# Performance work log

Measured on AMD Instinct MI355X. Metric: run time of the kernel, lower is better.

The kernel has to match this reference:

```python
import jax, jax.numpy as jnp
import numpy as np

N_NODES = 100000
N_EDGES = 1600000
IN_CH = 128
HID = 32
HEADS = 4
OUT_CH = 32
NEG_SLOPE = 0.2  # PyG GATConv default


def _gat_conv(x, src, dst, W, a_src, a_dst, bias, concat):
    """One GATConv layer (eval mode, self-loops already in src/dst).
    x: [N, F_in], W: [F_in, H*C], a_src/a_dst: [H, C], bias: [H*C] or [C].
    """
    N = x.shape[0]
    H, C = a_src.shape
    h = (x @ W).reshape(N, H, C)                      # [N, H, C]
    alpha_s = jnp.einsum('nhc,hc->nh', h, a_src)      # [N, H]
    alpha_d = jnp.einsum('nhc,hc->nh', h, a_dst)      # [N, H]
    logits = jax.nn.leaky_relu(alpha_s[src] + alpha_d[dst], NEG_SLOPE)  # [E, H]
    # segment softmax over incoming edges of each destination node
    m = jax.ops.segment_max(logits, dst, num_segments=N)   # [N, H]
    e = jnp.exp(logits - m[dst])                            # [E, H]
    denom = jax.ops.segment_sum(e, dst, num_segments=N)     # [N, H]
    alpha = e / denom[dst]                                   # [E, H]
    msg = h[src] * alpha[:, :, None]                         # [E, H, C]
    out = jax.ops.segment_sum(msg, dst, num_segments=N)     # [N, H, C]
    out = out.reshape(N, H * C) if concat else out.mean(axis=1)
    return out + bias


def setup_inputs() -> dict:
    key = jax.random.key(0)
    ks = jax.random.split(key, 12)
    x = jax.random.normal(ks[0], (N_NODES, IN_CH), dtype=jnp.float32)
    edge_index = jax.random.randint(ks[1], (2, N_EDGES), 0, N_NODES, dtype=jnp.int64)
    g = 0.1  # glorot-ish scale
    W1 = jax.random.normal(ks[2], (IN_CH, HEADS * HID), dtype=jnp.float32) * g
    a_src1 = jax.random.normal(ks[3], (HEADS, HID), dtype=jnp.float32) * g
    a_dst1 = jax.random.normal(ks[4], (HEADS, HID), dtype=jnp.float32) * g
    b1 = jnp.zeros((HEADS * HID,), dtype=jnp.float32)
    W2 = jax.random.normal(ks[5], (HEADS * HID, OUT_CH), dtype=jnp.float32) * g
    a_src2 = jax.random.normal(ks[6], (1, OUT_CH), dtype=jnp.float32) * g
    a_dst2 = jax.random.normal(ks[7], (1, OUT_CH), dtype=jnp.float32) * g
    b2 = jnp.zeros((OUT_CH,), dtype=jnp.float32)
    return {"x": x, "edge_index": edge_index,
            "W1": W1, "a_src1": a_src1, "a_dst1": a_dst1, "b1": b1,
            "W2": W2, "a_src2": a_src2, "a_dst2": a_dst2, "b2": b2}


def reference(x, edge_index, W1, a_src1, a_dst1, b1, W2, a_src2, a_dst2, b2):
    N = x.shape[0]
    loops = jnp.arange(N, dtype=edge_index.dtype)
    src = jnp.concatenate([edge_index[0], loops])  # add self-loops (PyG default)
    dst = jnp.concatenate([edge_index[1], loops])
    h = _gat_conv(x, src, dst, W1, a_src1, a_dst1, b1, concat=True)   # [N, H*HID]
    h = jax.nn.elu(h)
    out = _gat_conv(h, src, dst, W2, a_src2, a_dst2, b2, concat=False)  # [N, OUT]
    return out
```

## Files before the change

kernel.cpp:

```cpp
#include <hip/hip_runtime.h>
#include <math.h>

#define N_NODES 100000
#define N_EDGES 1600000
#define E_TOT   1700000
#define NEG_SLOPE 0.2f
#define NBUCK 196
#define G1_BLOCKS 1563
#define HISTB_BLOCKS 831

typedef unsigned short ushort_t;
typedef unsigned int uint_t;
typedef __attribute__((ext_vector_type(8))) short bf16x8;
typedef __attribute__((ext_vector_type(4))) float f32x4;

__device__ __forceinline__ float lrelu(float v) { return v > 0.f ? v : NEG_SLOPE * v; }
__device__ __forceinline__ float bf16lo(uint_t u) { return __uint_as_float(u << 16); }
__device__ __forceinline__ float bf16hi(uint_t u) { return __uint_as_float(u & 0xffff0000u); }
__device__ __forceinline__ ushort_t f2bf(float f) {
    uint_t u = __float_as_uint(f);
    u += 0x7fffu + ((u >> 16) & 1u);
    return (ushort_t)(u >> 16);
}

union BU { uint4 u; bf16x8 b; };

__global__ __launch_bounds__(256) void k_prep(const float* __restrict__ W,
                                              ushort_t* __restrict__ Wb,
                                              int* __restrict__ bucket_cnt)
{
    const int idx = blockIdx.x * 256 + threadIdx.x;
    if (blockIdx.x == 0 && threadIdx.x <= NBUCK) bucket_cnt[threadIdx.x] = 0;
    const int j  = idx & 7;
    const int kq = (idx >> 3) & 3;
    const int n  = (idx >> 5) & 15;
    const int tc = (idx >> 9) & 7;
    const int kc = idx >> 12;
    const int k = kc * 32 + kq * 8 + j;
    const int col = tc * 16 + n;
    Wb[idx] = f2bf(W[k * 128 + col]);
}

__global__ __launch_bounds__(256) void k_gemm1_histB(const float* __restrict__ x,
                                                     const ushort_t* __restrict__ Wb,
                                                     const float* __restrict__ a_src,
                                                     const float* __restrict__ a_dst,
                                                     ushort_t* __restrict__ hb,
                                                     float* __restrict__ as_,
                                                     float* __restrict__ ad_,
                                                     const int* __restrict__ ei,
                                                     int* __restrict__ bucket_cnt)
{
    __shared__ int lbin[NBUCK];
    const int t = threadIdx.x;

    if (blockIdx.x >= G1_BLOCKS) {
        const int e0 = (blockIdx.x - G1_BLOCKS) * 2048 + t;
        for (int i = t; i < NBUCK; i += 256) lbin[i] = 0;
        __syncthreads();
#pragma unroll
        for (int i = 0; i < 8; ++i) {
            const int e = e0 + i * 256;
            if (e < E_TOT) {
                const int d = (e < N_EDGES) ? ei[N_EDGES + e] : (e - N_EDGES);
                atomicAdd(&lbin[d >> 9], 1);
            }
        }
        __syncthreads();
        for (int i = t; i < NBUCK; i += 256)
            if (lbin[i]) atomicAdd(&bucket_cnt[i], lbin[i]);
        return;
    }

    const int lane = t & 63;
    const int w = t >> 6;
    const int rbase = blockIdx.x * 64 + w * 16;
    const int li = lane & 15;
    const int g = lane >> 4;

    f32x4 acc[8];
#pragma unroll
    for (int tc = 0; tc < 8; ++tc) acc[tc] = (f32x4){0.f, 0.f, 0.f, 0.f};

    int arow = rbase + li;
    if (arow > N_NODES - 1) arow = N_NODES - 1;
    const float* xr = x + (size_t)arow * 128 + g * 8;

#pragma unroll
    for (int kc = 0; kc < 4; ++kc) {
        const float4 a0 = *(const float4*)(xr + kc * 32);
        const float4 a1 = *(const float4*)(xr + kc * 32 + 4);
        BU au;
        au.u.x = (uint_t)f2bf(a0.x) | ((uint_t)f2bf(a0.y) << 16);
        au.u.y = (uint_t)f2bf(a0.z) | ((uint_t)f2bf(a0.w) << 16);
        au.u.z = (uint_t)f2bf(a1.x) | ((uint_t)f2bf(a1.y) << 16);
        au.u.w = (uint_t)f2bf(a1.z) | ((uint_t)f2bf(a1.w) << 16);
        const bf16x8 af = au.b;
#pragma unroll
        for (int tc = 0; tc < 8; ++tc) {
            const bf16x8 bf = *(const bf16x8*)(Wb + (size_t)(kc * 8 + tc) * 512 + li * 32 + g * 8);
            acc[tc] = __builtin_amdgcn_mfma_f32_16x16x32_bf16(af, bf, acc[tc], 0, 0, 0);
        }
    }

#pragma unroll
    for (int r = 0; r < 4; ++r) {
        const int row = rbase + g * 4 + r;
        if (row < N_NODES) {
            ushort_t* hp = hb + (size_t)row * 128 + li;
#pragma unroll
            for (int tc = 0; tc < 8; ++tc) hp[tc * 16] = f2bf(acc[tc][r]);
        }
    }

    float asv[8], adv[8];
#pragma unroll
    for (int tc = 0; tc < 8; ++tc) {
        asv[tc] = a_src[tc * 16 + li];
        adv[tc] = a_dst[tc * 16 + li];
    }
#pragma unroll
    for (int h = 0; h < 4; ++h) {
#pragma unroll
        for (int r = 0; r < 4; ++r) {
            float ps = acc[2 * h][r] * asv[2 * h] + acc[2 * h + 1][r] * asv[2 * h + 1];
            float pd = acc[2 * h][r] * adv[2 * h] + acc[2 * h + 1][r] * adv[2 * h + 1];
            ps += __shfl_xor(ps, 1); pd += __shfl_xor(pd, 1);
            ps += __shfl_xor(ps, 2); pd += __shfl_xor(pd, 2);
            ps += __shfl_xor(ps, 4); pd += __shfl_xor(pd, 4);
            ps += __shfl_xor(ps, 8); pd += __shfl_xor(pd, 8);
            const int row = rbase + g * 4 + r;
            if (li == 0 && row < N_NODES) {
                as_[row * 4 + h] = ps;
                ad_[row * 4 + h] = pd;
            }
        }
    }
}

__global__ __launch_bounds__(256) void k_scanB(const int* __restrict__ bucket_cnt,
                                               int* __restrict__ bucket_base,
                                               int* __restrict__ bucket_cursor)
{
    __shared__ int s[256];
    const int t = threadIdx.x;
    const int v = (t < NBUCK) ? bucket_cnt[t] : 0;
    s[t] = v; __syncthreads();
    for (int off = 1; off < 256; off <<= 1) {
        int a = (t >= off) ? s[t - off] : 0;
        __syncthreads();
        s[t] += a;
        __syncthreads();
    }
    const int excl = s[t] - v;
    if (t < NBUCK) {
        bucket_base[t] = excl;
        bucket_cursor[t] = excl;
        if (t == NBUCK - 1) bucket_base[NBUCK] = excl + v;
    }
}

__global__ __launch_bounds__(256) void k_scatterB(const int* __restrict__ ei,
                                                  int* __restrict__ bucket_cursor,
                                                  uint2* __restrict__ pairs)
{
    __shared__ int lcnt[NBUCK];
    __shared__ int lbase[NBUCK];
    const int t = threadIdx.x;
    const int e0 = blockIdx.x * 2048 + t;

    for (int i = t; i < NBUCK; i += 256) lcnt[i] = 0;
    __syncthreads();

    int s8[8], d8[8];
#pragma unroll
    for (int i = 0; i < 8; ++i) {
        const int e = e0 + i * 256;
        int s = -1, d = 0;
        if (e < E_TOT) {
            if (e < N_EDGES) { s = ei[e]; d = ei[N_EDGES + e]; }
            else { s = d = e - N_EDGES; }
            atomicAdd(&lcnt[d >> 9], 1);
        }
        s8[i] = s; d8[i] = d;
    }
    __syncthreads();
    for (int i = t; i < NBUCK; i += 256) {
        const int c = lcnt[i];
        lbase[i] = (c > 0) ? atomicAdd(&bucket_cursor[i], c) : 0;
    }
    __syncthreads();
    for (int i = t; i < NBUCK; i += 256) lcnt[i] = 0;
    __syncthreads();
#pragma unroll
    for (int i = 0; i < 8; ++i) {
        if (s8[i] >= 0) {
            const int b = d8[i] >> 9;
            const int pos = lbase[b] + atomicAdd(&lcnt[b], 1);
            pairs[pos] = make_uint2((uint_t)s8[i], (uint_t)d8[i]);
        }
    }
}

__global__ __launch_bounds__(256) void k_buildC(const uint2* __restrict__ pairs,
                                                const int* __restrict__ bucket_base,
                                                int* __restrict__ row_ptr,
                                                int* __restrict__ col_src)
{
    __shared__ int cnt[512];
    __shared__ int cur[512];
    __shared__ int ps[256];
    const int b = blockIdx.x, t = threadIdx.x;
    const int bstart = bucket_base[b], bend = bucket_base[b + 1];
    const int node0 = b << 9;

    cnt[t] = 0; cnt[t + 256] = 0;
    __syncthreads();
    for (int e = bstart + t; e < bend; e += 256)
        atomicAdd(&cnt[pairs[e].y - node0], 1);
    __syncthreads();

    const int pa = cnt[2 * t], pb = cnt[2 * t + 1];
    ps[t] = pa + pb; __syncthreads();
    for (int off = 1; off < 256; off <<= 1) {
        int a = (t >= off) ? ps[t - off] : 0;
        __syncthreads();
        ps[t] += a;
        __syncthreads();
    }
    const int pe = bstart + ps[t] - (pa + pb);
    cur[2 * t] = pe;
    cur[2 * t + 1] = pe + pa;
    const int n0 = node0 + 2 * t, n1 = node0 + 2 * t + 1;
    if (n0 < N_NODES) row_ptr[n0] = pe;
    if (n1 < N_NODES) row_ptr[n1] = pe + pa;
    if (b == 0 && t == 0) row_ptr[N_NODES] = E_TOT;
    __syncthreads();

    for (int e = bstart + t; e < bend; e += 256) {
        const uint2 pr = pairs[e];
        const int pos = atomicAdd(&cur[pr.y - node0], 1);
        col_src[pos] = (int)pr.x;
    }
}

__global__ __launch_bounds__(64) void k_agg1(const ushort_t* __restrict__ hb,
                                             const float* __restrict__ as_,
                                             const float* __restrict__ ad_,
                                             const int* __restrict__ row_ptr,
                                             const int* __restrict__ col_src,
                                             const float* __restrict__ bias,
                                             ushort_t* __restrict__ x2b)
{
    __shared__ float sEx[256];
    __shared__ int sSrc[64];
    const int n = blockIdx.x;
    const int lane = threadIdx.x;
    const int start = row_ptr[n], end = row_ptr[n + 1];
    const float4 adv = *(const float4*)(ad_ + (size_t)n * 4);

    const int hsel = lane >> 4;
    const int c0 = lane * 2;
    float2 acc = make_float2(0.f, 0.f);
    float4 ds = make_float4(0.f, 0.f, 0.f, 0.f);
    for (int base = start; base < end; base += 64) {
        const int e = base + lane;
        const int cnt = min(64, end - base);
        float4 ex = make_float4(0.f, 0.f, 0.f, 0.f);
        int s = 0;
        if (e < end) {
            s = col_src[e];
            const float4 av = *(const float4*)(as_ + (size_t)s * 4);
            ex.x = __expf(lrelu(av.x + adv.x));
            ex.y = __expf(lrelu(av.y + adv.y));
            ex.z = __expf(lrelu(av.z + adv.z));
            ex.w = __expf(lrelu(av.w + adv.w));
            ds.x += ex.x; ds.y += ex.y; ds.z += ex.z; ds.w += ex.w;
        }
        __syncthreads();
        *(float4*)(sEx + lane * 4) = ex;
        sSrc[lane] = s;
        __syncthreads();
        for (int i = 0; i < cnt; ++i) {
            const float w = sEx[i * 4 + hsel];
            const uint_t hv = *(const uint_t*)(hb + (size_t)sSrc[i] * 128 + c0);
            acc.x = fmaf(w, bf16lo(hv), acc.x);
            acc.y = fmaf(w, bf16hi(hv), acc.y);
        }
    }
#pragma unroll
    for (int off = 32; off > 0; off >>= 1) {
        ds.x += __shfl_xor(ds.x, off);
        ds.y += __shfl_xor(ds.y, off);
        ds.z += __shfl_xor(ds.z, off);
        ds.w += __shfl_xor(ds.w, off);
    }
    const float denom = hsel == 0 ? ds.x : hsel == 1 ? ds.y : hsel == 2 ? ds.z : ds.w;
    float o0 = acc.x / denom + bias[c0];
    float o1 = acc.y / denom + bias[c0 + 1];
    o0 = o0 > 0.f ? o0 : __expf(o0) - 1.f;
    o1 = o1 > 0.f ? o1 : __expf(o1) - 1.f;
    const uint_t q0 = f2bf(o0), q1 = f2bf(o1);
    *(uint_t*)(x2b + (size_t)n * 128 + c0) = q0 | (q1 << 16);
}

__global__ __launch_bounds__(256) void k_gemm2(const ushort_t* __restrict__ x2b,
                                               const float* __restrict__ W,
                                               const float* __restrict__ a_src,
                                               const float* __restrict__ a_dst,
                                               ushort_t* __restrict__ hb2,
                                               float* __restrict__ as_,
                                               float* __restrict__ ad_)
{
    __shared__ float sW[128 * 32];
    const int t = threadIdx.x;
    {
        const float4* W4 = (const float4*)W;
        float4* s4 = (float4*)sW;
#pragma unroll
        for (int i = 0; i < 4; ++i) s4[t + 256 * i] = W4[t + 256 * i];
    }
    __syncthreads();

    const int rr = t >> 5;
    const int c = t & 31;
    const float a_s = a_src[c], a_d = a_dst[c];

    for (int g = 0; g < 8; ++g) {
        const int row = blockIdx.x * 64 + g * 8 + rr;
        if (row >= N_NODES) continue;
        const ushort_t* xp = x2b + (size_t)row * 128;

        float acc = 0.f;
        for (int k = 0; k < 128; k += 4) {
            const uint2 u = *(const uint2*)(xp + k);
            acc = fmaf(bf16lo(u.x), sW[(k + 0) * 32 + c], acc);
            acc = fmaf(bf16hi(u.x), sW[(k + 1) * 32 + c], acc);
            acc = fmaf(bf16lo(u.y), sW[(k + 2) * 32 + c], acc);
            acc = fmaf(bf16hi(u.y), sW[(k + 3) * 32 + c], acc);
        }

        hb2[(size_t)row * 32 + c] = f2bf(acc);
        float ps = acc * a_s, pd = acc * a_d;
#pragma unroll
        for (int off = 16; off > 0; off >>= 1) {
            ps += __shfl_xor(ps, off);
            pd += __shfl_xor(pd, off);
        }
        if (c == 0) { as_[row] = ps; ad_[row] = pd; }
    }
}

__global__ __launch_bounds__(64) void k_agg2(const ushort_t* __restrict__ hb2,
                                             const float* __restrict__ as_,
                                             const float* __restrict__ ad_,
                                             const int* __restrict__ row_ptr,
                                             const int* __restrict__ col_src,
                                             const float* __restrict__ bias,
                                             float* __restrict__ out)
{
    __shared__ float sEx[64];
    __shared__ int sSrc[64];
    const int n = blockIdx.x;
    const int lane = threadIdx.x;
    const int start = row_ptr[n], end = row_ptr[n + 1];
    const float adn = ad_[n];

    const int c = lane & 31, half = lane >> 5;
    float acc = 0.f, dsum = 0.f;
    for (int base = start; base < end; base += 64) {
        const int e = base + lane;
        const int cnt = min(64, end - base);
        float ex = 0.f; int s = 0;
        if (e < end) {
            s = col_src[e];
            ex = __expf(lrelu(as_[s] + adn));
            dsum += ex;
        }
        __syncthreads();
        sEx[lane] = ex;
        sSrc[lane] = s;
        __syncthreads();
        for (int i = half; i < cnt; i += 2) {
            const ushort_t u = hb2[(size_t)sSrc[i] * 32 + c];
            acc = fmaf(sEx[i], __uint_as_float((uint_t)u << 16), acc);
        }
    }
#pragma unroll
    for (int off = 32; off > 0; off >>= 1) dsum += __shfl_xor(dsum, off);
    acc += __shfl_xor(acc, 32);
    if (half == 0) out[(size_t)n * 32 + c] = acc / dsum + bias[c];
}

extern "C" void kernel_launch(void* const* d_in, const int* in_sizes, int n_in,
                              void* d_out, int out_size, void* d_ws, size_t ws_size,
                              hipStream_t stream)
{
    const float* x      = (const float*)d_in[0];
    const int*   ei     = (const int*)d_in[1];
    const float* W1     = (const float*)d_in[2];
    const float* a_src1 = (const float*)d_in[3];
    const float* a_dst1 = (const float*)d_in[4];
    const float* b1     = (const float*)d_in[5];
    const float* W2     = (const float*)d_in[6];
    const float* a_src2 = (const float*)d_in[7];
    const float* a_dst2 = (const float*)d_in[8];
    const float* b2     = (const float*)d_in[9];
    float* out = (float*)d_out;

    char* p = (char*)d_ws;
    auto alloc = [&](size_t bytes) { char* q = p; p += (bytes + 255) & ~(size_t)255; return q; };
    ushort_t* h1b = (ushort_t*)alloc((size_t)N_NODES * 128 * 2);
    ushort_t* x2b = (ushort_t*)alloc((size_t)N_NODES * 128 * 2);
    ushort_t* h2b = (ushort_t*)alloc((size_t)N_NODES * 32 * 2);
    ushort_t* Wb  = (ushort_t*)alloc((size_t)16384 * 2);
    float* as1    = (float*)alloc((size_t)N_NODES * 4 * 4);
    float* ad1    = (float*)alloc((size_t)N_NODES * 4 * 4);
    float* as2    = (float*)alloc((size_t)N_NODES * 4);
    float* ad2    = (float*)alloc((size_t)N_NODES * 4);
    int* row_ptr  = (int*)alloc((size_t)(N_NODES + 1) * 4);
    int* bucket_cnt    = (int*)alloc((NBUCK + 1) * 4);
    int* bucket_base   = (int*)alloc((NBUCK + 1) * 4);
    int* bucket_cursor = (int*)alloc((NBUCK + 1) * 4);
    uint2* pairs  = (uint2*)alloc((size_t)E_TOT * 8);
    int* col_src  = (int*)alloc((size_t)E_TOT * 4);

    k_prep<<<64, 256, 0, stream>>>(W1, Wb, bucket_cnt);
    k_gemm1_histB<<<G1_BLOCKS + HISTB_BLOCKS, 256, 0, stream>>>(
        x, Wb, a_src1, a_dst1, h1b, as1, ad1, ei, bucket_cnt);
    k_scanB<<<1, 256, 0, stream>>>(bucket_cnt, bucket_base, bucket_cursor);
    k_scatterB<<<HISTB_BLOCKS, 256, 0, stream>>>(ei, bucket_cursor, pairs);
    k_buildC<<<NBUCK, 256, 0, stream>>>(pairs, bucket_base, row_ptr, col_src);
    k_agg1<<<N_NODES, 64, 0, stream>>>(h1b, as1, ad1, row_ptr, col_src, b1, x2b);
    k_gemm2<<<(N_NODES + 63) / 64, 256, 0, stream>>>(x2b, W2, a_src2, a_dst2, h2b, as2, ad2);
    k_agg2<<<N_NODES, 64, 0, stream>>>(h2b, as2, ad2, row_ptr, col_src, b2, out);
}
```

Measured before the change: 273.1 us.

## Fuse edge scatter into gemm1 launch and widen aggregation loads

The bucket histogram and scan now run as separate kernels ahead of gemm1, so the scatter pass can share a launch with gemm1 and overlap with it instead of running as its own kernel afterwards. The bucket counter is cleared with a memset. Both aggregation kernels now split edges across lane groups and load wider bf16 vectors per lane, followed by cross-lane shuffle reductions. This trades some extra shuffles and an extra small launch for fewer dependent serialized passes and better per-lane memory throughput.

```diff
diff --git a/kernel.cpp b/kernel.cpp
--- a/kernel.cpp
+++ b/kernel.cpp
@@ -7,7 +7,7 @@
 #define NEG_SLOPE 0.2f
 #define NBUCK 196
 #define G1_BLOCKS 1563
-#define HISTB_BLOCKS 831
+#define SCAT_BLOCKS 831
 
 typedef unsigned short ushort_t;
 typedef unsigned int uint_t;
@@ -25,12 +25,53 @@
 
 union BU { uint4 u; bf16x8 b; };
 
+__global__ __launch_bounds__(256) void k_histC(const int* __restrict__ ei,
+                                               int* __restrict__ bucket_cnt)
+{
+    __shared__ int lbin[NBUCK];
+    const int t = threadIdx.x;
+    const int e0 = blockIdx.x * 2048 + t;
+    for (int i = t; i < NBUCK; i += 256) lbin[i] = 0;
+    __syncthreads();
+#pragma unroll
+    for (int i = 0; i < 8; ++i) {
+        const int e = e0 + i * 256;
+        if (e < E_TOT) {
+            const int d = (e < N_EDGES) ? ei[N_EDGES + e] : (e - N_EDGES);
+            atomicAdd(&lbin[d >> 9], 1);
+        }
+    }
+    __syncthreads();
+    for (int i = t; i < NBUCK; i += 256)
+        if (lbin[i]) atomicAdd(&bucket_cnt[i], lbin[i]);
+}
+
+__global__ __launch_bounds__(256) void k_scanB(const int* __restrict__ bucket_cnt,
+                                               int* __restrict__ bucket_base,
+                                               int* __restrict__ bucket_cursor)
+{
+    __shared__ int s[256];
+    const int t = threadIdx.x;
+    const int v = (t < NBUCK) ? bucket_cnt[t] : 0;
+    s[t] = v; __syncthreads();
+    for (int off = 1; off < 256; off <<= 1) {
+        int a = (t >= off) ? s[t - off] : 0;
+        __syncthreads();
+        s[t] += a;
+        __syncthreads();
+    }
+    const int excl = s[t] - v;
+    if (t < NBUCK) {
+        bucket_base[t] = excl;
+        bucket_cursor[t] = excl;
+        if (t == NBUCK - 1) bucket_base[NBUCK] = excl + v;
+    }
+}
+
 __global__ __launch_bounds__(256) void k_prep(const float* __restrict__ W,
-                                              ushort_t* __restrict__ Wb,
-                                              int* __restrict__ bucket_cnt)
+                                              ushort_t* __restrict__ Wb)
 {
     const int idx = blockIdx.x * 256 + threadIdx.x;
-    if (blockIdx.x == 0 && threadIdx.x <= NBUCK) bucket_cnt[threadIdx.x] = 0;
     const int j  = idx & 7;
     const int kq = (idx >> 3) & 3;
     const int n  = (idx >> 5) & 15;
@@ -41,34 +82,53 @@
     Wb[idx] = f2bf(W[k * 128 + col]);
 }
 
-__global__ __launch_bounds__(256) void k_gemm1_histB(const float* __restrict__ x,
-                                                     const ushort_t* __restrict__ Wb,
-                                                     const float* __restrict__ a_src,
-                                                     const float* __restrict__ a_dst,
-                                                     ushort_t* __restrict__ hb,
-                                                     float* __restrict__ as_,
-                                                     float* __restrict__ ad_,
-                                                     const int* __restrict__ ei,
-                                                     int* __restrict__ bucket_cnt)
-{
-    __shared__ int lbin[NBUCK];
+__global__ __launch_bounds__(256) void k_gemm1_scat(const float* __restrict__ x,
+                                                    const ushort_t* __restrict__ Wb,
+                                                    const float* __restrict__ a_src,
+                                                    const float* __restrict__ a_dst,
+                                                    ushort_t* __restrict__ hb,
+                                                    float* __restrict__ as_,
+                                                    float* __restrict__ ad_,
+                                                    const int* __restrict__ ei,
+                                                    int* __restrict__ bucket_cursor,
+                                                    uint2* __restrict__ pairs)
+{
+    __shared__ int lcnt[NBUCK];
+    __shared__ int lbase[NBUCK];
     const int t = threadIdx.x;
 
     if (blockIdx.x >= G1_BLOCKS) {
         const int e0 = (blockIdx.x - G1_BLOCKS) * 2048 + t;
-        for (int i = t; i < NBUCK; i += 256) lbin[i] = 0;
-        __syncthreads();
+        for (int i = t; i < NBUCK; i += 256) lcnt[i] = 0;
+        __syncthreads();
+        int s8[8], d8[8];
 #pragma unroll
         for (int i = 0; i < 8; ++i) {
             const int e = e0 + i * 256;
+            int s = -1, d = 0;
             if (e < E_TOT) {
-                const int d = (e < N_EDGES) ? ei[N_EDGES + e] : (e - N_EDGES);
-                atomicAdd(&lbin[d >> 9], 1);
+                if (e < N_EDGES) { s = ei[e]; d = ei[N_EDGES + e]; }
+                else { s = d = e - N_EDGES; }
+                atomicAdd(&lcnt[d >> 9], 1);
             }
-        }
-        __syncthreads();
-        for (int i = t; i < NBUCK; i += 256)
-            if (lbin[i]) atomicAdd(&bucket_cnt[i], lbin[i]);
+            s8[i] = s; d8[i] = d;
+        }
+        __syncthreads();
+        for (int i = t; i < NBUCK; i += 256) {
+            const int c = lcnt[i];
+            lbase[i] = (c > 0) ? atomicAdd(&bucket_cursor[i], c) : 0;
+        }
+        __syncthreads();
+        for (int i = t; i < NBUCK; i += 256) lcnt[i] = 0;
+        __syncthreads();
+#pragma unroll
+        for (int i = 0; i < 8; ++i) {
+            if (s8[i] >= 0) {
+                const int b = d8[i] >> 9;
+                const int pos = lbase[b] + atomicAdd(&lcnt[b], 1);
+                pairs[pos] = make_uint2((uint_t)s8[i], (uint_t)d8[i]);
+            }
+        }
         return;
     }
 
@@ -138,70 +198,6 @@
     }
 }
 
-__global__ __launch_bounds__(256) void k_scanB(const int* __restrict__ bucket_cnt,
-                                               int* __restrict__ bucket_base,
-                                               int* __restrict__ bucket_cursor)
-{
-    __shared__ int s[256];
-    const int t = threadIdx.x;
-    const int v = (t < NBUCK) ? bucket_cnt[t] : 0;
-    s[t] = v; __syncthreads();
-    for (int off = 1; off < 256; off <<= 1) {
-        int a = (t >= off) ? s[t - off] : 0;
-        __syncthreads();
-        s[t] += a;
-        __syncthreads();
-    }
-    const int excl = s[t] - v;
-    if (t < NBUCK) {
-        bucket_base[t] = excl;
-        bucket_cursor[t] = excl;
-        if (t == NBUCK - 1) bucket_base[NBUCK] = excl + v;
-    }
-}
-
-__global__ __launch_bounds__(256) void k_scatterB(const int* __restrict__ ei,
-                                                  int* __restrict__ bucket_cursor,
-                                                  uint2* __restrict__ pairs)
-{
-    __shared__ int lcnt[NBUCK];
-    __shared__ int lbase[NBUCK];
-    const int t = threadIdx.x;
-    const int e0 = blockIdx.x * 2048 + t;
-
-    for (int i = t; i < NBUCK; i += 256) lcnt[i] = 0;
-    __syncthreads();
-
-    int s8[8], d8[8];
-#pragma unroll
-    for (int i = 0; i < 8; ++i) {
-        const int e = e0 + i * 256;
-        int s = -1, d = 0;
-        if (e < E_TOT) {
-            if (e < N_EDGES) { s = ei[e]; d = ei[N_EDGES + e]; }
-            else { s = d = e - N_EDGES; }
-            atomicAdd(&lcnt[d >> 9], 1);
-        }
-        s8[i] = s; d8[i] = d;
-    }
-    __syncthreads();
-    for (int i = t; i < NBUCK; i += 256) {
-        const int c = lcnt[i];
-        lbase[i] = (c > 0) ? atomicAdd(&bucket_cursor[i], c) : 0;
-    }
-    __syncthreads();
-    for (int i = t; i < NBUCK; i += 256) lcnt[i] = 0;
-    __syncthreads();
-#pragma unroll
-    for (int i = 0; i < 8; ++i) {
-        if (s8[i] >= 0) {
-            const int b = d8[i] >> 9;
-            const int pos = lbase[b] + atomicAdd(&lcnt[b], 1);
-            pairs[pos] = make_uint2((uint_t)s8[i], (uint_t)d8[i]);
-        }
-    }
-}
-
 __global__ __launch_bounds__(256) void k_buildC(const uint2* __restrict__ pairs,
                                                 const int* __restrict__ bucket_base,
                                                 int* __restrict__ row_ptr,
@@ -259,9 +255,12 @@
     const int start = row_ptr[n], end = row_ptr[n + 1];
     const float4 adv = *(const float4*)(ad_ + (size_t)n * 4);
 
-    const int hsel = lane >> 4;
-    const int c0 = lane * 2;
-    float2 acc = make_float2(0.f, 0.f);
+    const int half = lane >> 5;
+    const int cg = lane & 31;
+    const int c4 = cg * 4;
+    const int head = cg >> 3;
+
+    float4 acc = make_float4(0.f, 0.f, 0.f, 0.f);
     float4 ds = make_float4(0.f, 0.f, 0.f, 0.f);
     for (int base = start; base < end; base += 64) {
         const int e = base + lane;
@@ -281,11 +280,13 @@
         *(float4*)(sEx + lane * 4) = ex;
         sSrc[lane] = s;
         __syncthreads();
-        for (int i = 0; i < cnt; ++i) {
-            const float w = sEx[i * 4 + hsel];
-            const uint_t hv = *(const uint_t*)(hb + (size_t)sSrc[i] * 128 + c0);
-            acc.x = fmaf(w, bf16lo(hv), acc.x);
-            acc.y = fmaf(w, bf16hi(hv), acc.y);
+        for (int i = half; i < cnt; i += 2) {
+            const float w = sEx[i * 4 + head];
+            const uint2 hv = *(const uint2*)(hb + (size_t)sSrc[i] * 128 + c4);
+            acc.x = fmaf(w, bf16lo(hv.x), acc.x);
+            acc.y = fmaf(w, bf16hi(hv.x), acc.y);
+            acc.z = fmaf(w, bf16lo(hv.y), acc.z);
+            acc.w = fmaf(w, bf16hi(hv.y), acc.w);
         }
     }
 #pragma unroll
@@ -295,13 +296,25 @@
         ds.z += __shfl_xor(ds.z, off);
         ds.w += __shfl_xor(ds.w, off);
     }
-    const float denom = hsel == 0 ? ds.x : hsel == 1 ? ds.y : hsel == 2 ? ds.z : ds.w;
-    float o0 = acc.x / denom + bias[c0];
-    float o1 = acc.y / denom + bias[c0 + 1];
-    o0 = o0 > 0.f ? o0 : __expf(o0) - 1.f;
-    o1 = o1 > 0.f ? o1 : __expf(o1) - 1.f;
-    const uint_t q0 = f2bf(o0), q1 = f2bf(o1);
-    *(uint_t*)(x2b + (size_t)n * 128 + c0) = q0 | (q1 << 16);
+    acc.x += __shfl_xor(acc.x, 32);
+    acc.y += __shfl_xor(acc.y, 32);
+    acc.z += __shfl_xor(acc.z, 32);
+    acc.w += __shfl_xor(acc.w, 32);
+
+    if (half == 0) {
+        const float denom = head == 0 ? ds.x : head == 1 ? ds.y : head == 2 ? ds.z : ds.w;
+        const float4 b4 = *(const float4*)(bias + c4);
+        float o0 = acc.x / denom + b4.x;
+        float o1 = acc.y / denom + b4.y;
+        float o2 = acc.z / denom + b4.z;
+        float o3 = acc.w / denom + b4.w;
+        o0 = o0 > 0.f ? o0 : __expf(o0) - 1.f;
+        o1 = o1 > 0.f ? o1 : __expf(o1) - 1.f;
+        o2 = o2 > 0.f ? o2 : __expf(o2) - 1.f;
+        o3 = o3 > 0.f ? o3 : __expf(o3) - 1.f;
+        const uint_t q0 = f2bf(o0), q1 = f2bf(o1), q2 = f2bf(o2), q3 = f2bf(o3);
+        *(uint2*)(x2b + (size_t)n * 128 + c4) = make_uint2(q0 | (q1 << 16), q2 | (q3 << 16));
+    }
 }
 
 __global__ __launch_bounds__(256) void k_gemm2(const ushort_t* __restrict__ x2b,
@@ -366,8 +379,12 @@
     const int start = row_ptr[n], end = row_ptr[n + 1];
     const float adn = ad_[n];
 
-    const int c = lane & 31, half = lane >> 5;
-    float acc = 0.f, dsum = 0.f;
+    const int quarter = lane >> 4;
+    const int cg = lane & 15;
+    const int c2 = cg * 2;
+
+    float2 acc = make_float2(0.f, 0.f);
+    float dsum = 0.f;
     for (int base = start; base < end; base += 64) {
         const int e = base + lane;
         const int cnt = min(64, end - base);
@@ -381,15 +398,23 @@
         sEx[lane] = ex;
         sSrc[lane] = s;
         __syncthreads();
-        for (int i = half; i < cnt; i += 2) {
-            const ushort_t u = hb2[(size_t)sSrc[i] * 32 + c];
-            acc = fmaf(sEx[i], __uint_as_float((uint_t)u << 16), acc);
+        for (int i = quarter; i < cnt; i += 4) {
+            const float w = sEx[i];
+            const uint_t hv = *(const uint_t*)(hb2 + (size_t)sSrc[i] * 32 + c2);
+            acc.x = fmaf(w, bf16lo(hv), acc.x);
+            acc.y = fmaf(w, bf16hi(hv), acc.y);
         }
     }
 #pragma unroll
     for (int off = 32; off > 0; off >>= 1) dsum += __shfl_xor(dsum, off);
-    acc += __shfl_xor(acc, 32);
-    if (half == 0) out[(size_t)n * 32 + c] = acc / dsum + bias[c];
+    acc.x += __shfl_xor(acc.x, 16);
+    acc.y += __shfl_xor(acc.y, 16);
+    acc.x += __shfl_xor(acc.x, 32);
+    acc.y += __shfl_xor(acc.y, 32);
+    if (quarter == 0) {
+        float2 o = make_float2(acc.x / dsum + bias[c2], acc.y / dsum + bias[c2 + 1]);
+        *(float2*)(out + (size_t)n * 32 + c2) = o;
+    }
 }
 
 extern "C" void kernel_launch(void* const* d_in, const int* in_sizes, int n_in,
@@ -425,11 +450,13 @@
     uint2* pairs  = (uint2*)alloc((size_t)E_TOT * 8);
     int* col_src  = (int*)alloc((size_t)E_TOT * 4);
 
-    k_prep<<<64, 256, 0, stream>>>(W1, Wb, bucket_cnt);
-    k_gemm1_histB<<<G1_BLOCKS + HISTB_BLOCKS, 256, 0, stream>>>(
-        x, Wb, a_src1, a_dst1, h1b, as1, ad1, ei, bucket_cnt);
+    (void)hipMemsetAsync(bucket_cnt, 0, (NBUCK + 1) * 4, stream);
+
+    k_histC<<<SCAT_BLOCKS, 256, 0, stream>>>(ei, bucket_cnt);
     k_scanB<<<1, 256, 0, stream>>>(bucket_cnt, bucket_base, bucket_cursor);
-    k_scatterB<<<HISTB_BLOCKS, 256, 0, stream>>>(ei, bucket_cursor, pairs);
+    k_prep<<<64, 256, 0, stream>>>(W1, Wb);
+    k_gemm1_scat<<<G1_BLOCKS + SCAT_BLOCKS, 256, 0, stream>>>(
+        x, Wb, a_src1, a_dst1, h1b, as1, ad1, ei, bucket_cursor, pairs);
     k_buildC<<<NBUCK, 256, 0, stream>>>(pairs, bucket_base, row_ptr, col_src);
     k_agg1<<<N_NODES, 64, 0, stream>>>(h1b, as1, ad1, row_ptr, col_src, b1, x2b);
     k_gemm2<<<(N_NODES + 63) / 64, 256, 0, stream>>>(x2b, W2, a_src2, a_dst2, h2b, as2, ad2);
```

New measurement: 265.1 us. 1.03x faster.

## Move histogram into prep kernel and fuse scatter with GEMM1 launch

Applied to the files above, without the earlier changes.

The destination histogram now runs inside the W1 bf16 conversion kernel, and the bucket scatter runs as extra blocks of the GEMM1 kernel. This drops one launch and lets the scatter work overlap with the dense GEMM instead of running after it. The bucket counter is now zeroed with a memset, which adds a small async op. buildC moves to 512 threads with one node per thread, which simplifies its scan but makes the scan loop longer.

```diff
diff --git a/kernel.cpp b/kernel.cpp
--- a/kernel.cpp
+++ b/kernel.cpp
@@ -7,7 +7,8 @@
 #define NEG_SLOPE 0.2f
 #define NBUCK 196
 #define G1_BLOCKS 1563
-#define HISTB_BLOCKS 831
+#define SCAT_BLOCKS 831
+#define PREP_BLOCKS 64
 
 typedef unsigned short ushort_t;
 typedef unsigned int uint_t;
@@ -25,50 +26,110 @@
 
 union BU { uint4 u; bf16x8 b; };
 
-__global__ __launch_bounds__(256) void k_prep(const float* __restrict__ W,
-                                              ushort_t* __restrict__ Wb,
-                                              int* __restrict__ bucket_cnt)
-{
-    const int idx = blockIdx.x * 256 + threadIdx.x;
-    if (blockIdx.x == 0 && threadIdx.x <= NBUCK) bucket_cnt[threadIdx.x] = 0;
-    const int j  = idx & 7;
-    const int kq = (idx >> 3) & 3;
-    const int n  = (idx >> 5) & 15;
-    const int tc = (idx >> 9) & 7;
-    const int kc = idx >> 12;
-    const int k = kc * 32 + kq * 8 + j;
-    const int col = tc * 16 + n;
-    Wb[idx] = f2bf(W[k * 128 + col]);
-}
-
-__global__ __launch_bounds__(256) void k_gemm1_histB(const float* __restrict__ x,
-                                                     const ushort_t* __restrict__ Wb,
-                                                     const float* __restrict__ a_src,
-                                                     const float* __restrict__ a_dst,
-                                                     ushort_t* __restrict__ hb,
-                                                     float* __restrict__ as_,
-                                                     float* __restrict__ ad_,
-                                                     const int* __restrict__ ei,
-                                                     int* __restrict__ bucket_cnt)
+__global__ __launch_bounds__(256) void k_prep_hist(const float* __restrict__ W,
+                                                   ushort_t* __restrict__ Wb,
+                                                   const int* __restrict__ ei,
+                                                   int* __restrict__ bucket_cnt)
 {
     __shared__ int lbin[NBUCK];
     const int t = threadIdx.x;
 
+    if (blockIdx.x < PREP_BLOCKS) {
+        const int idx = blockIdx.x * 256 + t;
+        const int j  = idx & 7;
+        const int kq = (idx >> 3) & 3;
+        const int n  = (idx >> 5) & 15;
+        const int tc = (idx >> 9) & 7;
+        const int kc = idx >> 12;
+        Wb[idx] = f2bf(W[(kc * 32 + kq * 8 + j) * 128 + tc * 16 + n]);
+        return;
+    }
+
+    const int e0 = (blockIdx.x - PREP_BLOCKS) * 2048 + t;
+    for (int i = t; i < NBUCK; i += 256) lbin[i] = 0;
+    __syncthreads();
+#pragma unroll
+    for (int i = 0; i < 8; ++i) {
+        const int e = e0 + i * 256;
+        if (e < E_TOT) {
+            const int d = (e < N_EDGES) ? ei[N_EDGES + e] : (e - N_EDGES);
+            atomicAdd(&lbin[d >> 9], 1);
+        }
+    }
+    __syncthreads();
+    for (int i = t; i < NBUCK; i += 256)
+        if (lbin[i]) atomicAdd(&bucket_cnt[i], lbin[i]);
+}
+
+__global__ __launch_bounds__(256) void k_scanB(const int* __restrict__ bucket_cnt,
+                                               int* __restrict__ bucket_base,
+                                               int* __restrict__ bucket_cursor)
+{
+    __shared__ int s[256];
+    const int t = threadIdx.x;
+    const int v = (t < NBUCK) ? bucket_cnt[t] : 0;
+    s[t] = v; __syncthreads();
+    for (int off = 1; off < 256; off <<= 1) {
+        int a = (t >= off) ? s[t - off] : 0;
+        __syncthreads();
+        s[t] += a;
+        __syncthreads();
+    }
+    const int excl = s[t] - v;
+    if (t < NBUCK) {
+        bucket_base[t] = excl;
+        bucket_cursor[t] = excl;
+        if (t == NBUCK - 1) bucket_base[NBUCK] = excl + v;
+    }
+}
+
+__global__ __launch_bounds__(256) void k_gemm1_scat(const float* __restrict__ x,
+                                                    const ushort_t* __restrict__ Wb,
+                                                    const float* __restrict__ a_src,
+                                                    const float* __restrict__ a_dst,
+                                                    ushort_t* __restrict__ hb,
+                                                    float* __restrict__ as_,
+                                                    float* __restrict__ ad_,
+                                                    const int* __restrict__ ei,
+                                                    int* __restrict__ bucket_cursor,
+                                                    uint2* __restrict__ pairs)
+{
+    __shared__ int lcnt[NBUCK];
+    __shared__ int lbase[NBUCK];
+    const int t = threadIdx.x;
+
     if (blockIdx.x >= G1_BLOCKS) {
         const int e0 = (blockIdx.x - G1_BLOCKS) * 2048 + t;
-        for (int i = t; i < NBUCK; i += 256) lbin[i] = 0;
-        __syncthreads();
+        for (int i = t; i < NBUCK; i += 256) lcnt[i] = 0;
+        __syncthreads();
+        int s8[8], d8[8];
 #pragma unroll
         for (int i = 0; i < 8; ++i) {
             const int e = e0 + i * 256;
+            int s = -1, d = 0;
             if (e < E_TOT) {
-                const int d = (e < N_EDGES) ? ei[N_EDGES + e] : (e - N_EDGES);
-                atomicAdd(&lbin[d >> 9], 1);
+                if (e < N_EDGES) { s = ei[e]; d = ei[N_EDGES + e]; }
+                else { s = d = e - N_EDGES; }
+                atomicAdd(&lcnt[d >> 9], 1);
             }
-        }
-        __syncthreads();
-        for (int i = t; i < NBUCK; i += 256)
-            if (lbin[i]) atomicAdd(&bucket_cnt[i], lbin[i]);
+            s8[i] = s; d8[i] = d;
+        }
+        __syncthreads();
+        for (int i = t; i < NBUCK; i += 256) {
+            const int c = lcnt[i];
+            lbase[i] = (c > 0) ? atomicAdd(&bucket_cursor[i], c) : 0;
+        }
+        __syncthreads();
+        for (int i = t; i < NBUCK; i += 256) lcnt[i] = 0;
+        __syncthreads();
+#pragma unroll
+        for (int i = 0; i < 8; ++i) {
+            if (s8[i] >= 0) {
+                const int b = d8[i] >> 9;
+                const int pos = lbase[b] + atomicAdd(&lcnt[b], 1);
+                pairs[pos] = make_uint2((uint_t)s8[i], (uint_t)d8[i]);
+            }
+        }
         return;
     }
 
@@ -138,106 +199,39 @@
     }
 }
 
-__global__ __launch_bounds__(256) void k_scanB(const int* __restrict__ bucket_cnt,
-                                               int* __restrict__ bucket_base,
-                                               int* __restrict__ bucket_cursor)
-{
-    __shared__ int s[256];
-    const int t = threadIdx.x;
-    const int v = (t < NBUCK) ? bucket_cnt[t] : 0;
-    s[t] = v; __syncthreads();
-    for (int off = 1; off < 256; off <<= 1) {
-        int a = (t >= off) ? s[t - off] : 0;
-        __syncthreads();
-        s[t] += a;
-        __syncthreads();
-    }
-    const int excl = s[t] - v;
-    if (t < NBUCK) {
-        bucket_base[t] = excl;
-        bucket_cursor[t] = excl;
-        if (t == NBUCK - 1) bucket_base[NBUCK] = excl + v;
-    }
-}
-
-__global__ __launch_bounds__(256) void k_scatterB(const int* __restrict__ ei,
-                                                  int* __restrict__ bucket_cursor,
-                                                  uint2* __restrict__ pairs)
-{
-    __shared__ int lcnt[NBUCK];
-    __shared__ int lbase[NBUCK];
-    const int t = threadIdx.x;
-    const int e0 = blockIdx.x * 2048 + t;
-
-    for (int i = t; i < NBUCK; i += 256) lcnt[i] = 0;
-    __syncthreads();
-
-    int s8[8], d8[8];
-#pragma unroll
-    for (int i = 0; i < 8; ++i) {
-        const int e = e0 + i * 256;
-        int s = -1, d = 0;
-        if (e < E_TOT) {
-            if (e < N_EDGES) { s = ei[e]; d = ei[N_EDGES + e]; }
-            else { s = d = e - N_EDGES; }
-            atomicAdd(&lcnt[d >> 9], 1);
-        }
-        s8[i] = s; d8[i] = d;
-    }
-    __syncthreads();
-    for (int i = t; i < NBUCK; i += 256) {
-        const int c = lcnt[i];
-        lbase[i] = (c > 0) ? atomicAdd(&bucket_cursor[i], c) : 0;
-    }
-    __syncthreads();
-    for (int i = t; i < NBUCK; i += 256) lcnt[i] = 0;
-    __syncthreads();
-#pragma unroll
-    for (int i = 0; i < 8; ++i) {
-        if (s8[i] >= 0) {
-            const int b = d8[i] >> 9;
-            const int pos = lbase[b] + atomicAdd(&lcnt[b], 1);
-            pairs[pos] = make_uint2((uint_t)s8[i], (uint_t)d8[i]);
-        }
-    }
-}
-
-__global__ __launch_bounds__(256) void k_buildC(const uint2* __restrict__ pairs,
+__global__ __launch_bounds__(512) void k_buildC(const uint2* __restrict__ pairs,
                                                 const int* __restrict__ bucket_base,
                                                 int* __restrict__ row_ptr,
                                                 int* __restrict__ col_src)
 {
     __shared__ int cnt[512];
     __shared__ int cur[512];
-    __shared__ int ps[256];
     const int b = blockIdx.x, t = threadIdx.x;
     const int bstart = bucket_base[b], bend = bucket_base[b + 1];
     const int node0 = b << 9;
 
-    cnt[t] = 0; cnt[t + 256] = 0;
-    __syncthreads();
-    for (int e = bstart + t; e < bend; e += 256)
+    cnt[t] = 0;
+    __syncthreads();
+    for (int e = bstart + t; e < bend; e += 512)
         atomicAdd(&cnt[pairs[e].y - node0], 1);
     __syncthreads();
 
-    const int pa = cnt[2 * t], pb = cnt[2 * t + 1];
-    ps[t] = pa + pb; __syncthreads();
-    for (int off = 1; off < 256; off <<= 1) {
-        int a = (t >= off) ? ps[t - off] : 0;
-        __syncthreads();
-        ps[t] += a;
-        __syncthreads();
-    }
-    const int pe = bstart + ps[t] - (pa + pb);
-    cur[2 * t] = pe;
-    cur[2 * t + 1] = pe + pa;
-    const int n0 = node0 + 2 * t, n1 = node0 + 2 * t + 1;
-    if (n0 < N_NODES) row_ptr[n0] = pe;
-    if (n1 < N_NODES) row_ptr[n1] = pe + pa;
+    const int v = cnt[t];
+    cur[t] = v; __syncthreads();
+    for (int off = 1; off < 512; off <<= 1) {
+        int a = (t >= off) ? cur[t - off] : 0;
+        __syncthreads();
+        cur[t] += a;
+        __syncthreads();
+    }
+    const int excl = bstart + cur[t] - v;
+    const int node = node0 + t;
+    if (node < N_NODES) row_ptr[node] = excl;
     if (b == 0 && t == 0) row_ptr[N_NODES] = E_TOT;
-    __syncthreads();
-
-    for (int e = bstart + t; e < bend; e += 256) {
+    cur[t] = excl;
+    __syncthreads();
+
+    for (int e = bstart + t; e < bend; e += 512) {
         const uint2 pr = pairs[e];
         const int pos = atomicAdd(&cur[pr.y - node0], 1);
         col_src[pos] = (int)pr.x;
@@ -425,12 +419,13 @@
     uint2* pairs  = (uint2*)alloc((size_t)E_TOT * 8);
     int* col_src  = (int*)alloc((size_t)E_TOT * 4);
 
-    k_prep<<<64, 256, 0, stream>>>(W1, Wb, bucket_cnt);
-    k_gemm1_histB<<<G1_BLOCKS + HISTB_BLOCKS, 256, 0, stream>>>(
-        x, Wb, a_src1, a_dst1, h1b, as1, ad1, ei, bucket_cnt);
+    (void)hipMemsetAsync(bucket_cnt, 0, (NBUCK + 1) * 4, stream);
+
+    k_prep_hist<<<PREP_BLOCKS + SCAT_BLOCKS, 256, 0, stream>>>(W1, Wb, ei, bucket_cnt);
     k_scanB<<<1, 256, 0, stream>>>(bucket_cnt, bucket_base, bucket_cursor);
-    k_scatterB<<<HISTB_BLOCKS, 256, 0, stream>>>(ei, bucket_cursor, pairs);
-    k_buildC<<<NBUCK, 256, 0, stream>>>(pairs, bucket_base, row_ptr, col_src);
+    k_gemm1_scat<<<G1_BLOCKS + SCAT_BLOCKS, 256, 0, stream>>>(
+        x, Wb, a_src1, a_dst1, h1b, as1, ad1, ei, bucket_cursor, pairs);
+    k_buildC<<<NBUCK, 512, 0, stream>>>(pairs, bucket_base, row_ptr, col_src);
     k_agg1<<<N_NODES, 64, 0, stream>>>(h1b, as1, ad1, row_ptr, col_src, b1, x2b);
     k_gemm2<<<(N_NODES + 63) / 64, 256, 0, stream>>>(x2b, W2, a_src2, a_dst2, h2b, as2, ad2);
     k_agg2<<<N_NODES, 64, 0, stream>>>(h2b, as2, ad2, row_ptr, col_src, b2, out);
```

New measurement: 266.6 us. 2.4% less time.
